# Performance work log

Hardware: AMD Instinct MI355X
Metric: run time of the kernel (lower is better)

Reference implementation:

```python
import math
import jax, jax.numpy as jnp
import numpy as np

FEAT = (32, 96, 96)   # feature-space D,H,W (image 128x384x384 at scale 4)
C_IN = 256
DIM = 48              # patch_dim
PS = 24               # patch_size = instance_crop_size // feature_scale
SIG = 1024
POS = (8, 8, 8, 4)    # pos_emb_shape
N = 64                # num instances
SCALE = 4
CROP = 96


def setup_inputs() -> dict:
    key = jax.random.key(0)
    ks = jax.random.split(key, 16)
    def w(k, shape, s=0.02):
        return jax.random.normal(k, shape, dtype=jnp.float32) * s
    feature = jax.random.normal(ks[0], FEAT + (C_IN,), dtype=jnp.float32)
    # locations in original-image pixel coordinates
    locations = jax.random.uniform(ks[1], (N, 3), dtype=jnp.float32) * jnp.asarray(
        [FEAT[0] * SCALE, FEAT[1] * SCALE, FEAT[2] * SCALE], jnp.float32)
    return dict(
        feature=feature, locations=locations,
        conv0_w=w(ks[2], (3, 3, 3, C_IN, DIM)), conv0_b=jnp.zeros((DIM,), jnp.float32),
        conv1_w=w(ks[3], (3, 3, 3, DIM, DIM)), conv1_b=jnp.zeros((DIM,), jnp.float32),
        ca_w=w(ks[4], (DIM, DIM)), ca_b=jnp.zeros((DIM,), jnp.float32),
        sig_w=w(ks[5], (4 * 4 * 4 * DIM, SIG)), sig_b=jnp.zeros((SIG,), jnp.float32),
        ln_scale=jnp.ones((SIG,), jnp.float32), ln_bias=jnp.zeros((SIG,), jnp.float32),
        pe1_w=w(ks[6], (SIG, SIG)), pe1_b=jnp.zeros((SIG,), jnp.float32),
        pe2_w=w(ks[7], (SIG, SIG)), pe2_b=jnp.zeros((SIG,), jnp.float32),
        pe3_w=w(ks[8], (SIG, math.prod(POS))), pe3_b=jnp.zeros((math.prod(POS),), jnp.float32),
        pe_proj_w=w(ks[9], (POS[-1], DIM)),
        ct_w=w(ks[10], (2, 2, 2, DIM, 1)), ct_b=jnp.zeros((1,), jnp.float32),
    )


def _conv3d(x, w, b):
    y = jax.lax.conv_general_dilated(x[None], w, (1, 1, 1), 'SAME',
        dimension_numbers=('NDHWC', 'DHWIO', 'NDHWC'))[0]
    return y + b


def _forward(feature, locations, conv0_w, conv0_b, conv1_w, conv1_b, ca_w, ca_b,
             sig_w, sig_b, ln_scale, ln_bias, pe1_w, pe1_b, pe2_w, pe2_b,
             pe3_w, pe3_b, pe_proj_w, ct_w, ct_b):
    n = locations.shape[0]
    locs = locations / SCALE
    # feature mixing convs
    x = jax.nn.gelu(_conv3d(feature, conv0_w, conv0_b))
    x = _conv3d(x, conv1_w, conv1_b)                       # [D,H,W,DIM]
    # _get_patch: gather PS^3 sub-volumes at N locations with bounds masking
    loc0 = locs.astype(jnp.int32) - PS // 2                 # [N,3] top-left corners
    grid = jnp.mgrid[:PS, :PS, :PS]                         # [3,PS,PS,PS]
    coords = grid[None] + loc0[:, :, None, None, None]      # [N,3,PS,PS,PS]
    limit = jnp.asarray(x.shape[:-1]).reshape(1, 3, 1, 1, 1)
    valid = (coords >= 0).all(axis=1) & (coords < limit).all(axis=1)  # [N,PS,PS,PS]
    patches = jnp.where(valid[..., None],
                        x[coords[:, 0], coords[:, 1], coords[:, 2]], 0.0)
    # ChannelAttention (SE-style: global pool -> dense -> sigmoid gate)
    gate = jax.nn.sigmoid(patches.mean(axis=(1, 2, 3)) @ ca_w + ca_b)  # [N,DIM]
    patches = patches * gate[:, None, None, None, :]
    # _get_signiture
    bw = PS // 4
    inner = patches[:, bw:-bw, bw:-bw, bw:-bw, :]
    s = jax.image.resize(inner, (n, 4, 4, 4, DIM), 'linear').reshape(n, -1)
    s = s @ sig_w + sig_b
    mu = s.mean(-1, keepdims=True)
    var = ((s - mu) ** 2).mean(-1, keepdims=True)
    patch_sigs = (s - mu) * jax.lax.rsqrt(var + 1e-6) * ln_scale + ln_bias
    # _add_pos_encoding
    p = jax.nn.gelu(patch_sigs @ pe1_w + pe1_b)
    p = jax.nn.gelu(p @ pe2_w + pe2_b)
    p = p @ pe3_w + pe3_b                                   # [N, prod(POS)]
    p = jax.image.resize(p.reshape(-1, *POS), (n, PS, PS, PS, POS[-1]), 'linear')
    patches = jax.nn.relu(patches + p @ pe_proj_w)          # [N,PS,PS,PS,DIM]
    # decode: ConvTranspose x2 then trilinear resize to full crop
    logits = jax.lax.conv_transpose(patches, ct_w, (2, 2, 2), 'SAME',
        dimension_numbers=('NDHWC', 'DHWIO', 'NDHWC')) + ct_b  # [N,2PS,2PS,2PS,1]
    logits = jax.image.resize(logits[..., 0], (n, CROP, CROP, CROP), 'linear')
    mask = locs[:, -1] >= 0
    plocs = jnp.where(mask[:, None], loc0 * SCALE, -1)
    return patch_sigs, logits, plocs[:, 0], plocs[:, 1], plocs[:, 2], mask


def reference(feature, locations, conv0_w, conv0_b, conv1_w, conv1_b, ca_w, ca_b,
              sig_w, sig_b, ln_scale, ln_bias, pe1_w, pe1_b, pe2_w, pe2_b,
              pe3_w, pe3_b, pe_proj_w, ct_w, ct_b):
    return _forward(feature, locations, conv0_w, conv0_b, conv1_w, conv1_b, ca_w,
                    ca_b, sig_w, sig_b, ln_scale, ln_bias, pe1_w, pe1_b, pe2_w,
                    pe2_b, pe3_w, pe3_b, pe_proj_w, ct_w, ct_b)
```

## Files before the change

kernel.cpp:

```cpp
#include <hip/hip_runtime.h>
#include <hip/hip_bf16.h>
#include <math.h>


#define NLOC 64

typedef __attribute__((ext_vector_type(8))) short short8_t;
typedef __attribute__((ext_vector_type(4))) float f32x4;

__device__ __forceinline__ float gelu_f(float x) {
    return 0.5f * x * (1.0f + tanhf(0.7978845608028654f * (x + 0.044715f * x * x * x)));
}

__device__ __forceinline__ short f2bf(float x) {
    union { __hip_bfloat16 h; short s; } u;
    u.h = __float2bfloat16(x);
    return u.s;
}

__constant__ float W12c[4][12] = {
    {0.25f, 0.375f, 0.25f, 0.125f, 0.f, 0.f, 0.f, 0.f, 0.f, 0.f, 0.f, 0.f},
    {0.f, 0.f, 1.f/9.f, 2.f/9.f, 1.f/3.f, 2.f/9.f, 1.f/9.f, 0.f, 0.f, 0.f, 0.f, 0.f},
    {0.f, 0.f, 0.f, 0.f, 0.f, 1.f/9.f, 2.f/9.f, 1.f/3.f, 2.f/9.f, 1.f/9.f, 0.f, 0.f},
    {0.f, 0.f, 0.f, 0.f, 0.f, 0.f, 0.f, 0.f, 0.125f, 0.25f, 0.375f, 0.25f}};

__device__ __forceinline__ void up_w(int i, float ratio, int inmax,
                                     int& j0, int& j1, float& w0, float& w1) {
    float c = ((float)i + 0.5f) * ratio - 0.5f;
    float fj = floorf(c);
    float f = c - fj;
    int jj = (int)fj;
    j0 = min(max(jj, 0), inmax);
    j1 = min(max(jj + 1, 0), inmax);
    w0 = 1.f - f;
    w1 = f;
}

__global__ void prep_w0_kernel(const float* __restrict__ w0, short* __restrict__ wf) {
    const int tid = blockIdx.x * 256 + threadIdx.x;
    if (tid >= 27 * 8 * 3 * 64) return;
    const int lane = tid & 63;
    const int t2 = tid >> 6;
    const int nt = t2 % 3;
    const int t3 = t2 / 3;
    const int kk = t3 & 7, tap = t3 >> 3;
    const int g = lane >> 4, rr = lane & 15;
    const int co = nt * 16 + rr;
    short8_t frag;
#pragma unroll
    for (int e = 0; e < 8; e++) {
        const int ci = kk * 32 + g * 8 + e;
        frag[e] = f2bf(w0[((long)(tap * 256 + ci)) * 48 + co]);
    }
    ((short8_t*)wf)[tid] = frag;
}

__global__ void prep_w1_kernel(const float* __restrict__ w1, short* __restrict__ wf) {
    const int tid = blockIdx.x * 256 + threadIdx.x;
    if (tid >= 27 * 2 * 3 * 64) return;
    const int lane = tid & 63;
    const int t2 = tid >> 6;
    const int nt = t2 % 3;
    const int t3 = t2 / 3;
    const int kk = t3 & 1, tap = t3 >> 1;
    const int g = lane >> 4, rr = lane & 15;
    const int co = nt * 16 + rr;
    short8_t frag;
#pragma unroll
    for (int e = 0; e < 8; e++) {
        const int ci = kk * 32 + g * 8 + e;
        frag[e] = (ci < 48) ? f2bf(w1[((long)(tap * 48 + ci)) * 48 + co]) : (short)0;
    }
    ((short8_t*)wf)[tid] = frag;
}

#define HV 600
#define HSTR 40

__global__ __launch_bounds__(256) void conv0_mfma(const float* __restrict__ feat,
                                                  const short* __restrict__ wf,
                                                  const float* __restrict__ bias,
                                                  short* __restrict__ x0b) {
    __shared__ short slds[HV * HSTR];
    const int tid = threadIdx.x;
    const int lane = tid & 63, wid = tid >> 6;
    const int g = lane >> 4, r = lane & 15;
    const int bz = blockIdx.x / 144, by = (blockIdx.x / 12) % 12, bx = blockIdx.x % 12;
    const int z0 = bz * 4, y0 = by * 8, x0c = bx * 8;
    int h0[4];
#pragma unroll
    for (int mt = 0; mt < 4; mt++) {
        const int t = wid * 64 + mt * 16 + r;
        h0[mt] = ((t >> 6) * 10 + ((t >> 3) & 7)) * 10 + (t & 7);
    }
    f32x4 acc[4][3];
#pragma unroll
    for (int mt = 0; mt < 4; mt++)
#pragma unroll
        for (int nt = 0; nt < 3; nt++) acc[mt][nt] = (f32x4){0.f, 0.f, 0.f, 0.f};
    const short8_t zfrag = {0, 0, 0, 0, 0, 0, 0, 0};
    const short8_t* wf8 = (const short8_t*)wf;

    for (int kk = 0; kk < 8; kk++) {
        __syncthreads();
        for (int h = tid; h < HV; h += 256) {
            const int hx = h % 10, hy = (h / 10) % 10, hz = h / 100;
            const int zz = z0 + hz - 1, yy = y0 + hy - 1, xx = x0c + hx - 1;
            short8_t s8[4];
            if ((unsigned)zz < 32u && (unsigned)yy < 96u && (unsigned)xx < 96u) {
                const float4* src =
                    (const float4*)(feat + (((((long)zz * 96 + yy) * 96 + xx)) << 8) + kk * 32);
#pragma unroll
                for (int q = 0; q < 4; q++) {
                    const float4 a = src[2 * q], b = src[2 * q + 1];
                    s8[q][0] = f2bf(a.x); s8[q][1] = f2bf(a.y);
                    s8[q][2] = f2bf(a.z); s8[q][3] = f2bf(a.w);
                    s8[q][4] = f2bf(b.x); s8[q][5] = f2bf(b.y);
                    s8[q][6] = f2bf(b.z); s8[q][7] = f2bf(b.w);
                }
            } else {
#pragma unroll
                for (int q = 0; q < 4; q++) s8[q] = zfrag;
            }
            short8_t* dst = (short8_t*)(slds + h * HSTR);
#pragma unroll
            for (int q = 0; q < 4; q++) dst[q] = s8[q];
        }
        __syncthreads();
        for (int tap = 0; tap < 27; tap++) {
            const int dh = (tap / 9) * 100 + ((tap / 3) % 3) * 10 + (tap % 3);
            short8_t bfr[3];
#pragma unroll
            for (int nt = 0; nt < 3; nt++)
                bfr[nt] = wf8[(size_t)tap * 1536 + kk * 192 + nt * 64 + lane];
            short8_t afr[4];
#pragma unroll
            for (int mt = 0; mt < 4; mt++)
                afr[mt] = *(const short8_t*)(slds + (h0[mt] + dh) * HSTR + g * 8);
#pragma unroll
            for (int mt = 0; mt < 4; mt++)
#pragma unroll
                for (int nt = 0; nt < 3; nt++)
                    acc[mt][nt] = __builtin_amdgcn_mfma_f32_16x16x32_bf16(afr[mt], bfr[nt],
                                                                          acc[mt][nt], 0, 0, 0);
        }
    }
#pragma unroll
    for (int nt = 0; nt < 3; nt++) {
        const int co = nt * 16 + r;
        const float bv = bias[co];
#pragma unroll
        for (int mt = 0; mt < 4; mt++) {
#pragma unroll
            for (int rg = 0; rg < 4; rg++) {
                const int t = wid * 64 + mt * 16 + g * 4 + rg;
                const int z = z0 + (t >> 6), y = y0 + ((t >> 3) & 7), x = x0c + (t & 7);
                const long gi = ((long)z * 96 + y) * 96 + x;
                x0b[gi * 48 + co] = f2bf(gelu_f(acc[mt][nt][rg] + bv));
            }
        }
    }
}

#define C1ROW 48

__global__ __launch_bounds__(256, 1) void conv1_mfma_b(const short* __restrict__ x0b,
                                                       const short* __restrict__ wf,
                                                       const float* __restrict__ bias,
                                                       float* __restrict__ x1) {
    __shared__ short slds[HV * C1ROW];
    const int tid = threadIdx.x;
    const int lane = tid & 63, wid = tid >> 6;
    const int g = lane >> 4, r = lane & 15;
    const int bz = blockIdx.x / 144, by = (blockIdx.x / 12) % 12, bx = blockIdx.x % 12;
    const int z0 = bz * 4, y0 = by * 8, x0c = bx * 8;
    int h0[4];
#pragma unroll
    for (int mt = 0; mt < 4; mt++) {
        const int t = wid * 64 + mt * 16 + r;
        h0[mt] = ((t >> 6) * 10 + ((t >> 3) & 7)) * 10 + (t & 7);
    }
    f32x4 acc[4][3];
#pragma unroll
    for (int mt = 0; mt < 4; mt++)
#pragma unroll
        for (int nt = 0; nt < 3; nt++) acc[mt][nt] = (f32x4){0.f, 0.f, 0.f, 0.f};
    const short8_t zfrag = {0, 0, 0, 0, 0, 0, 0, 0};
    const short8_t* wf8 = (const short8_t*)wf;

    for (int h = tid; h < HV; h += 256) {
        const int hx = h % 10, hy = (h / 10) % 10, hz = h / 100;
        const int zz = z0 + hz - 1, yy = y0 + hy - 1, xx = x0c + hx - 1;
        short8_t s8[6];
        if ((unsigned)zz < 32u && (unsigned)yy < 96u && (unsigned)xx < 96u) {
            const short8_t* src = (const short8_t*)(x0b + (((long)zz * 96 + yy) * 96 + xx) * 48);
#pragma unroll
            for (int q = 0; q < 6; q++) s8[q] = src[q];
        } else {
#pragma unroll
            for (int q = 0; q < 6; q++) s8[q] = zfrag;
        }
        short8_t* dst = (short8_t*)(slds + h * C1ROW);
#pragma unroll
        for (int q = 0; q < 6; q++) dst[q] = s8[q];
    }
    __syncthreads();

    for (int tap = 0; tap < 27; tap++) {
        const int dh = (tap / 9) * 100 + ((tap / 3) % 3) * 10 + (tap % 3);
#pragma unroll
        for (int kk = 0; kk < 2; kk++) {
            short8_t bfr[3];
#pragma unroll
            for (int nt = 0; nt < 3; nt++)
                bfr[nt] = wf8[(size_t)tap * 384 + kk * 192 + nt * 64 + lane];
            short8_t afr[4];
#pragma unroll
            for (int mt = 0; mt < 4; mt++) {
                afr[mt] = zfrag;
                if (!(kk == 1 && g >= 2))
                    afr[mt] =
                        *(const short8_t*)(slds + (h0[mt] + dh) * C1ROW + kk * 32 + g * 8);
            }
#pragma unroll
            for (int mt = 0; mt < 4; mt++)
#pragma unroll
                for (int nt = 0; nt < 3; nt++)
                    acc[mt][nt] = __builtin_amdgcn_mfma_f32_16x16x32_bf16(afr[mt], bfr[nt],
                                                                          acc[mt][nt], 0, 0, 0);
        }
    }
#pragma unroll
    for (int nt = 0; nt < 3; nt++) {
        const int co = nt * 16 + r;
        const float bv = bias[co];
#pragma unroll
        for (int mt = 0; mt < 4; mt++) {
#pragma unroll
            for (int rg = 0; rg < 4; rg++) {
                const int t = wid * 64 + mt * 16 + g * 4 + rg;
                const int z = z0 + (t >> 6), y = y0 + ((t >> 3) & 7), x = x0c + (t & 7);
                const long gi = ((long)z * 96 + y) * 96 + x;
                x1[gi * 48 + co] = acc[mt][nt][rg] + bv;
            }
        }
    }
}

__global__ __launch_bounds__(256) void mean_part_kernel(const float* __restrict__ x1,
                                                        const float* __restrict__ locations,
                                                        float* __restrict__ part) {
    __shared__ float red[256];
    const int n = blockIdx.x, i = blockIdx.y;
    const int tid = threadIdx.x;
    const int ch = tid & 63, grp = tid >> 6;
    const int lz = (int)(locations[n * 3 + 0] * 0.25f) - 12;
    const int ly = (int)(locations[n * 3 + 1] * 0.25f) - 12;
    const int lx = (int)(locations[n * 3 + 2] * 0.25f) - 12;
    float acc = 0.f;
    const int z = lz + i;
    if (ch < 48 && (unsigned)z < 32u) {
        for (int p = grp; p < 576; p += 4) {
            const int j = p / 24, k = p % 24;
            const int y = ly + j, x = lx + k;
            if ((unsigned)y < 96u && (unsigned)x < 96u)
                acc += x1[(((long)z * 96 + y) * 96 + x) * 48 + ch];
        }
    }
    red[tid] = acc;
    __syncthreads();
    if (tid < 48)
        part[(n * 24 + i) * 48 + tid] = red[tid] + red[tid + 64] + red[tid + 128] + red[tid + 192];
}

__global__ void gate_kernel(const float* __restrict__ part, const float* __restrict__ caw,
                            const float* __restrict__ cab, float* __restrict__ gate) {
    __shared__ float sm[48];
    const int n = blockIdx.x, t = threadIdx.x;
    if (t < 48) {
        float a = 0.f;
        for (int i = 0; i < 24; i++) a += part[(n * 24 + i) * 48 + t];
        sm[t] = a * (1.f / 13824.f);
    }
    __syncthreads();
    if (t < 48) {
        float g = cab[t];
        for (int c = 0; c < 48; c++) g += sm[c] * caw[c * 48 + t];
        gate[n * 48 + t] = 1.f / (1.f + expf(-g));
    }
}

__global__ __launch_bounds__(256) void rs1_kernel(const float* __restrict__ x1,
                                                  const float* __restrict__ locations,
                                                  const float* __restrict__ gate,
                                                  float* __restrict__ t1) {
    const int idx = blockIdx.x * 256 + threadIdx.x;
    int ch = idx % 48;
    int r = idx / 48;
    int c4 = r & 3; r >>= 2;
    int j = r % 12; r /= 12;
    int i = r % 12;
    int n = r / 12;
    const int lz = (int)(locations[n * 3 + 0] * 0.25f) - 6;
    const int ly = (int)(locations[n * 3 + 1] * 0.25f) - 6;
    const int lx = (int)(locations[n * 3 + 2] * 0.25f) - 6;
    const int z = lz + i, y = ly + j;
    float acc = 0.f;
    if ((unsigned)z < 32u && (unsigned)y < 96u) {
        const float* row = x1 + (((long)z * 96 + y) * 96) * 48 + ch;
#pragma unroll
        for (int k = 0; k < 12; k++) {
            const int x = lx + k;
            if ((unsigned)x < 96u) acc += W12c[c4][k] * row[(long)x * 48];
        }
    }
    t1[idx] = acc * gate[n * 48 + ch];
}

__global__ __launch_bounds__(256) void rs2_kernel(const float* __restrict__ t1,
                                                  float* __restrict__ t2) {
    const int idx = blockIdx.x * 256 + threadIdx.x;
    int ch = idx % 48;
    int r = idx / 48;
    int c = r & 3; r >>= 2;
    int b = r & 3; r >>= 2;
    int i = r % 12;
    int n = r / 12;
    float acc = 0.f;
#pragma unroll
    for (int j = 0; j < 12; j++)
        acc += W12c[b][j] * t1[(((long)((n * 12 + i) * 12 + j) * 4 + c)) * 48 + ch];
    t2[idx] = acc;
}

__global__ __launch_bounds__(256) void rs3_kernel(const float* __restrict__ t2,
                                                  float* __restrict__ rs) {
    const int idx = blockIdx.x * 256 + threadIdx.x;
    int ch = idx % 48;
    int r = idx / 48;
    int c = r & 3; r >>= 2;
    int b = r & 3; r >>= 2;
    int a = r & 3;
    int n = r >> 2;
    float acc = 0.f;
#pragma unroll
    for (int i = 0; i < 12; i++)
        acc += W12c[a][i] * t2[(((long)((n * 12 + i) * 4 + b) * 4 + c)) * 48 + ch];
    rs[idx] = acc;
}

template <int K, bool GEL>
__global__ __launch_bounds__(256) void mlp_kernel(const float* __restrict__ A,
                                                  const float* __restrict__ W,
                                                  const float* __restrict__ bias,
                                                  float* __restrict__ C, int N) {
    const int n = threadIdx.x & 63;
    const int j = blockIdx.x * 4 + (threadIdx.x >> 6);
    float acc = bias[j];
    const float* a = A + (long)n * K;
    const float* wp = W + j;
    for (int k = 0; k < K; k++) acc += a[k] * wp[(long)k * N];
    if (GEL) acc = gelu_f(acc);
    C[(long)n * N + j] = acc;
}

__global__ __launch_bounds__(256) void ln_kernel(const float* __restrict__ s,
                                                 const float* __restrict__ sc,
                                                 const float* __restrict__ bi,
                                                 float* __restrict__ out) {
    __shared__ float red[256];
    const int n = blockIdx.x, tid = threadIdx.x;
    float4 v = ((const float4*)(s + (long)n * 1024))[tid];
    red[tid] = v.x + v.y + v.z + v.w;
    __syncthreads();
    for (int off = 128; off > 0; off >>= 1) {
        if (tid < off) red[tid] += red[tid + off];
        __syncthreads();
    }
    const float mu = red[0] * (1.f / 1024.f);
    __syncthreads();
    const float d0 = v.x - mu, d1 = v.y - mu, d2 = v.z - mu, d3 = v.w - mu;
    red[tid] = d0 * d0 + d1 * d1 + d2 * d2 + d3 * d3;
    __syncthreads();
    for (int off = 128; off > 0; off >>= 1) {
        if (tid < off) red[tid] += red[tid + off];
        __syncthreads();
    }
    const float rstd = rsqrtf(red[0] * (1.f / 1024.f) + 1e-6f);
    const int base = n * 1024 + tid * 4;
    out[base + 0] = d0 * rstd * sc[tid * 4 + 0] + bi[tid * 4 + 0];
    out[base + 1] = d1 * rstd * sc[tid * 4 + 1] + bi[tid * 4 + 1];
    out[base + 2] = d2 * rstd * sc[tid * 4 + 2] + bi[tid * 4 + 2];
    out[base + 3] = d3 * rstd * sc[tid * 4 + 3] + bi[tid * 4 + 3];
}

__global__ __launch_bounds__(256) void deconv_kernel(const float* __restrict__ x1,
                                                     const float* __restrict__ locations,
                                                     const float* __restrict__ gate,
                                                     const float* __restrict__ p3,
                                                     const float* __restrict__ projw,
                                                     const float* __restrict__ ctw,
                                                     const float* __restrict__ ctb,
                                                     float* __restrict__ l48) {
    __shared__ float s_ctw[384], s_proj[192], s_gate[48];
    const int n = blockIdx.y, tid = threadIdx.x;
    for (int i = tid; i < 384; i += 256) s_ctw[i] = ctw[i];
    if (tid < 192) s_proj[tid] = projw[tid];
    if (tid < 48) s_gate[tid] = gate[n * 48 + tid];
    __syncthreads();
    const int vox = blockIdx.x * 256 + tid;
    const int q = vox % 24, pp = (vox / 24) % 24, m = vox / 576;
    const int lz = (int)(locations[n * 3 + 0] * 0.25f) - 12;
    const int ly = (int)(locations[n * 3 + 1] * 0.25f) - 12;
    const int lx = (int)(locations[n * 3 + 2] * 0.25f) - 12;
    const int z = lz + m, y = ly + pp, x = lx + q;
    float pf[48];
    const bool valid = (unsigned)z < 32u && (unsigned)y < 96u && (unsigned)x < 96u;
    if (valid) {
        const float4* src = (const float4*)(x1 + (((long)z * 96 + y) * 96 + x) * 48);
#pragma unroll
        for (int t = 0; t < 12; t++) {
            float4 v = src[t];
            pf[t * 4 + 0] = v.x * s_gate[t * 4 + 0];
            pf[t * 4 + 1] = v.y * s_gate[t * 4 + 1];
            pf[t * 4 + 2] = v.z * s_gate[t * 4 + 2];
            pf[t * 4 + 3] = v.w * s_gate[t * 4 + 3];
        }
    } else {
#pragma unroll
        for (int c = 0; c < 48; c++) pf[c] = 0.f;
    }
    int jz[2], jy[2], jx[2];
    float wz[2], wy[2], wx[2];
    const float r3 = 1.f / 3.f;
    up_w(m, r3, 7, jz[0], jz[1], wz[0], wz[1]);
    up_w(pp, r3, 7, jy[0], jy[1], wy[0], wy[1]);
    up_w(q, r3, 7, jx[0], jx[1], wx[0], wx[1]);
    const float4* prow = (const float4*)(p3 + (long)n * 2048);
    float prx = 0.f, pry = 0.f, prz = 0.f, prw = 0.f;
#pragma unroll
    for (int a = 0; a < 2; a++)
#pragma unroll
        for (int b = 0; b < 2; b++)
#pragma unroll
            for (int c = 0; c < 2; c++) {
                const float wgt = wz[a] * wy[b] * wx[c];
                float4 v = prow[(jz[a] * 8 + jy[b]) * 8 + jx[c]];
                prx += wgt * v.x;
                pry += wgt * v.y;
                prz += wgt * v.z;
                prw += wgt * v.w;
            }
#pragma unroll
    for (int c = 0; c < 48; c++) {
        float v = pf[c] + prx * s_proj[c] + pry * s_proj[48 + c] + prz * s_proj[96 + c] +
                  prw * s_proj[144 + c];
        pf[c] = fmaxf(v, 0.f);
    }
    const float bias = ctb[0];
#pragma unroll
    for (int a = 0; a < 2; a++)
#pragma unroll
        for (int b = 0; b < 2; b++)
#pragma unroll
            for (int c = 0; c < 2; c++) {
                const float* wrow = s_ctw + (((1 - a) * 2 + (1 - b)) * 2 + (1 - c)) * 48;
                float acc = bias;
#pragma unroll
                for (int ch = 0; ch < 48; ch++) acc += pf[ch] * wrow[ch];
                l48[(((long)n * 48 + 2 * m + a) * 48 + 2 * pp + b) * 48 + 2 * q + c] = acc;
            }
}

__global__ __launch_bounds__(256) void resize96_kernel(const float* __restrict__ l48,
                                                       float* __restrict__ out) {
    const int n = blockIdx.y;
    const int vox = blockIdx.x * 256 + threadIdx.x;
    const int kx = vox % 96, jy = (vox / 96) % 96, iz = vox / 9216;
    int a0, a1, b0, b1, c0, c1;
    float wa0, wa1, wb0, wb1, wc0, wc1;
    up_w(iz, 0.5f, 47, a0, a1, wa0, wa1);
    up_w(jy, 0.5f, 47, b0, b1, wb0, wb1);
    up_w(kx, 0.5f, 47, c0, c1, wc0, wc1);
    const float* base = l48 + (long)n * 110592;
    const float v =
        wa0 * (wb0 * (wc0 * base[(a0 * 48 + b0) * 48 + c0] + wc1 * base[(a0 * 48 + b0) * 48 + c1]) +
               wb1 * (wc0 * base[(a0 * 48 + b1) * 48 + c0] + wc1 * base[(a0 * 48 + b1) * 48 + c1])) +
        wa1 * (wb0 * (wc0 * base[(a1 * 48 + b0) * 48 + c0] + wc1 * base[(a1 * 48 + b0) * 48 + c1]) +
               wb1 * (wc0 * base[(a1 * 48 + b1) * 48 + c0] + wc1 * base[(a1 * 48 + b1) * 48 + c1]));
    out[(long)n * 884736 + vox] = v;
}

__global__ void tail_kernel(const float* __restrict__ locations, float* __restrict__ out) {
    const int n = threadIdx.x;
    if (n < NLOC) {
        const float l0 = locations[n * 3 + 0] * 0.25f;
        const float l1 = locations[n * 3 + 1] * 0.25f;
        const float l2 = locations[n * 3 + 2] * 0.25f;
        const int z = (int)l0 - 12, y = (int)l1 - 12, x = (int)l2 - 12;
        const bool mask = (l2 >= 0.f);
        out[n] = mask ? (float)(z * 4) : -1.f;
        out[64 + n] = mask ? (float)(y * 4) : -1.f;
        out[128 + n] = mask ? (float)(x * 4) : -1.f;
        out[192 + n] = mask ? 1.f : 0.f;
    }
}

static const size_t OFF_X0 = 0;
static const size_t OFF_X1 = 14155776;
static const size_t OFF_WF0 = 14155776;
static const size_t OFF_GATE = 4096;
static const size_t OFF_T1 = 8192;
static const size_t OFF_T2 = 1777664;
static const size_t OFF_RS = 2367488;
static const size_t OFF_S = 2564096;
static const size_t OFF_P1 = 2629632;
static const size_t OFF_P2 = 2695168;
static const size_t OFF_P3 = 2760704;
static const size_t OFF_L48 = 2891776;
static const size_t OFF_PART = 10000000;

static const size_t OUT_WF1 = 65536;

extern "C" void kernel_launch(void* const* d_in, const int* in_sizes, int n_in,
                              void* d_out, int out_size, void* d_ws, size_t ws_size,
                              hipStream_t stream) {
    const float* feature = (const float*)d_in[0];
    const float* locations = (const float*)d_in[1];
    const float* w0 = (const float*)d_in[2];
    const float* b0 = (const float*)d_in[3];
    const float* w1 = (const float*)d_in[4];
    const float* b1 = (const float*)d_in[5];
    const float* caw = (const float*)d_in[6];
    const float* cab = (const float*)d_in[7];
    const float* sigw = (const float*)d_in[8];
    const float* sigb = (const float*)d_in[9];
    const float* lnsc = (const float*)d_in[10];
    const float* lnbi = (const float*)d_in[11];
    const float* pe1w = (const float*)d_in[12];
    const float* pe1b = (const float*)d_in[13];
    const float* pe2w = (const float*)d_in[14];
    const float* pe2b = (const float*)d_in[15];
    const float* pe3w = (const float*)d_in[16];
    const float* pe3b = (const float*)d_in[17];
    const float* projw = (const float*)d_in[18];
    const float* ctw = (const float*)d_in[19];
    const float* ctb = (const float*)d_in[20];
    float* ws = (float*)d_ws;
    float* out = (float*)d_out;

    short* x0b = (short*)(ws + OFF_X0);
    float* x1 = ws + OFF_X1;
    short* wf0 = (short*)(ws + OFF_WF0);
    short* wf1 = (short*)(out + OUT_WF1);

    prep_w0_kernel<<<162, 256, 0, stream>>>(w0, wf0);
    prep_w1_kernel<<<41, 256, 0, stream>>>(w1, wf1);

    conv0_mfma<<<1152, 256, 0, stream>>>(feature, wf0, b0, x0b);
    conv1_mfma_b<<<1152, 256, 0, stream>>>(x0b, wf1, b1, x1);

    mean_part_kernel<<<dim3(64, 24), 256, 0, stream>>>(x1, locations, ws + OFF_PART);
    gate_kernel<<<64, 64, 0, stream>>>(ws + OFF_PART, caw, cab, ws + OFF_GATE);

    rs1_kernel<<<6912, 256, 0, stream>>>(x1, locations, ws + OFF_GATE, ws + OFF_T1);
    rs2_kernel<<<2304, 256, 0, stream>>>(ws + OFF_T1, ws + OFF_T2);
    rs3_kernel<<<768, 256, 0, stream>>>(ws + OFF_T2, ws + OFF_RS);

    mlp_kernel<3072, false><<<256, 256, 0, stream>>>(ws + OFF_RS, sigw, sigb, ws + OFF_S, 1024);
    ln_kernel<<<64, 256, 0, stream>>>(ws + OFF_S, lnsc, lnbi, out);

    mlp_kernel<1024, true><<<256, 256, 0, stream>>>(out, pe1w, pe1b, ws + OFF_P1, 1024);
    mlp_kernel<1024, true><<<256, 256, 0, stream>>>(ws + OFF_P1, pe2w, pe2b, ws + OFF_P2, 1024);
    mlp_kernel<1024, false><<<512, 256, 0, stream>>>(ws + OFF_P2, pe3w, pe3b, ws + OFF_P3, 2048);

    deconv_kernel<<<dim3(54, 64), 256, 0, stream>>>(x1, locations, ws + OFF_GATE, ws + OFF_P3,
                                                    projw, ctw, ctb, ws + OFF_L48);

    resize96_kernel<<<dim3(3456, 64), 256, 0, stream>>>(ws + OFF_L48, out + 65536);

    tail_kernel<<<1, 64, 0, stream>>>(locations, out + 56688640);
}
```

Before: 1.246 ms.

## Prefetch next channel chunk into registers during MFMA loop in conv0

```diff
diff --git a/kernel.cpp b/kernel.cpp
--- a/kernel.cpp
+++ b/kernel.cpp
@@ -101,32 +101,106 @@
     const short8_t zfrag = {0, 0, 0, 0, 0, 0, 0, 0};
     const short8_t* wf8 = (const short8_t*)wf;
 
+    bool v1, v2, v3 = false;
+    const float *p1, *p2, *p3 = feat;
+    {
+        const int h = tid;
+        const int hx = h % 10, hy = (h / 10) % 10, hz = h / 100;
+        const int zz = z0 + hz - 1, yy = y0 + hy - 1, xx = x0c + hx - 1;
+        v1 = (unsigned)zz < 32u && (unsigned)yy < 96u && (unsigned)xx < 96u;
+        p1 = feat + (v1 ? ((((long)zz * 96 + yy) * 96 + xx) << 8) : 0);
+    }
+    {
+        const int h = tid + 256;
+        const int hx = h % 10, hy = (h / 10) % 10, hz = h / 100;
+        const int zz = z0 + hz - 1, yy = y0 + hy - 1, xx = x0c + hx - 1;
+        v2 = (unsigned)zz < 32u && (unsigned)yy < 96u && (unsigned)xx < 96u;
+        p2 = feat + (v2 ? ((((long)zz * 96 + yy) * 96 + xx) << 8) : 0);
+    }
+    if (tid < 88) {
+        const int h = tid + 512;
+        const int hx = h % 10, hy = (h / 10) % 10, hz = h / 100;
+        const int zz = z0 + hz - 1, yy = y0 + hy - 1, xx = x0c + hx - 1;
+        v3 = (unsigned)zz < 32u && (unsigned)yy < 96u && (unsigned)xx < 96u;
+        p3 = feat + (v3 ? ((((long)zz * 96 + yy) * 96 + xx) << 8) : 0);
+    }
+
+    if (!v1) {
+        short8_t* d = (short8_t*)(slds + tid * HSTR);
+#pragma unroll
+        for (int q = 0; q < 4; q++) d[q] = zfrag;
+    }
+    if (!v2) {
+        short8_t* d = (short8_t*)(slds + (tid + 256) * HSTR);
+#pragma unroll
+        for (int q = 0; q < 4; q++) d[q] = zfrag;
+    }
+    if (tid < 88 && !v3) {
+        short8_t* d = (short8_t*)(slds + (tid + 512) * HSTR);
+#pragma unroll
+        for (int q = 0; q < 4; q++) d[q] = zfrag;
+    }
+
+    float4 pre1[8], pre2[8];
+    if (v1) {
+        const float4* s = (const float4*)p1;
+#pragma unroll
+        for (int q = 0; q < 8; q++) pre1[q] = s[q];
+    }
+    if (v2) {
+        const float4* s = (const float4*)p2;
+#pragma unroll
+        for (int q = 0; q < 8; q++) pre2[q] = s[q];
+    }
+
     for (int kk = 0; kk < 8; kk++) {
+        if (v1) {
+            short8_t* d = (short8_t*)(slds + tid * HSTR);
+#pragma unroll
+            for (int q = 0; q < 4; q++) {
+                const float4 a = pre1[2 * q], b = pre1[2 * q + 1];
+                short8_t s8;
+                s8[0] = f2bf(a.x); s8[1] = f2bf(a.y); s8[2] = f2bf(a.z); s8[3] = f2bf(a.w);
+                s8[4] = f2bf(b.x); s8[5] = f2bf(b.y); s8[6] = f2bf(b.z); s8[7] = f2bf(b.w);
+                d[q] = s8;
+            }
+        }
+        if (v2) {
+            short8_t* d = (short8_t*)(slds + (tid + 256) * HSTR);
+#pragma unroll
+            for (int q = 0; q < 4; q++) {
+                const float4 a = pre2[2 * q], b = pre2[2 * q + 1];
+                short8_t s8;
+                s8[0] = f2bf(a.x); s8[1] = f2bf(a.y); s8[2] = f2bf(a.z); s8[3] = f2bf(a.w);
+                s8[4] = f2bf(b.x); s8[5] = f2bf(b.y); s8[6] = f2bf(b.z); s8[7] = f2bf(b.w);
+                d[q] = s8;
+            }
+        }
+        if (tid < 88 && v3) {
+            const float4* s = (const float4*)(p3 + kk * 32);
+            short8_t* d = (short8_t*)(slds + (tid + 512) * HSTR);
+#pragma unroll
+            for (int q = 0; q < 4; q++) {
+                const float4 a = s[2 * q], b = s[2 * q + 1];
+                short8_t s8;
+                s8[0] = f2bf(a.x); s8[1] = f2bf(a.y); s8[2] = f2bf(a.z); s8[3] = f2bf(a.w);
+                s8[4] = f2bf(b.x); s8[5] = f2bf(b.y); s8[6] = f2bf(b.z); s8[7] = f2bf(b.w);
+                d[q] = s8;
+            }
+        }
         __syncthreads();
-        for (int h = tid; h < HV; h += 256) {
-            const int hx = h % 10, hy = (h / 10) % 10, hz = h / 100;
-            const int zz = z0 + hz - 1, yy = y0 + hy - 1, xx = x0c + hx - 1;
-            short8_t s8[4];
-            if ((unsigned)zz < 32u && (unsigned)yy < 96u && (unsigned)xx < 96u) {
-                const float4* src =
-                    (const float4*)(feat + (((((long)zz * 96 + yy) * 96 + xx)) << 8) + kk * 32);
-#pragma unroll
-                for (int q = 0; q < 4; q++) {
-                    const float4 a = src[2 * q], b = src[2 * q + 1];
-                    s8[q][0] = f2bf(a.x); s8[q][1] = f2bf(a.y);
-                    s8[q][2] = f2bf(a.z); s8[q][3] = f2bf(a.w);
-                    s8[q][4] = f2bf(b.x); s8[q][5] = f2bf(b.y);
-                    s8[q][6] = f2bf(b.z); s8[q][7] = f2bf(b.w);
-                }
-            } else {
-#pragma unroll
-                for (int q = 0; q < 4; q++) s8[q] = zfrag;
-            }
-            short8_t* dst = (short8_t*)(slds + h * HSTR);
-#pragma unroll
-            for (int q = 0; q < 4; q++) dst[q] = s8[q];
-        }
-        __syncthreads();
+        if (kk < 7) {
+            if (v1) {
+                const float4* s = (const float4*)(p1 + (kk + 1) * 32);
+#pragma unroll
+                for (int q = 0; q < 8; q++) pre1[q] = s[q];
+            }
+            if (v2) {
+                const float4* s = (const float4*)(p2 + (kk + 1) * 32);
+#pragma unroll
+                for (int q = 0; q < 8; q++) pre2[q] = s[q];
+            }
+        }
         for (int tap = 0; tap < 27; tap++) {
             const int dh = (tap / 9) * 100 + ((tap / 3) % 3) * 10 + (tap % 3);
             short8_t bfr[3];
@@ -144,6 +218,7 @@
                     acc[mt][nt] = __builtin_amdgcn_mfma_f32_16x16x32_bf16(afr[mt], bfr[nt],
                                                                           acc[mt][nt], 0, 0, 0);
         }
+        __syncthreads();
     }
 #pragma unroll
     for (int nt = 0; nt < 3; nt++) {
```

Result: no change. 1.262 ms (+1.2%).
